# Kernel tuning notes

Hardware: AMD Instinct MI355X
Metric: run time of the kernel (lower is better)

The kernel has to match this reference:

```python
import jax, jax.numpy as jnp
import numpy as np


def pan_conv(x, edge_index, filter_w, lin_w, lin_b):
    """Faithful dense equivalent of PANConv.

    panentropy: pan = w0*I + w1*A + w2*A^2 (filter_size terms).
    PyG then extracts nonzero edges (row=source j, col=target i), computes
    deg = count of pan-edges per row, norm = deg^-1/2[row]*deg^-1/2[col],
    and scatter-adds norm*edge_weight*x_j at target i. Dense form:
      out = d[:,None] * (pan.T @ (d[:,None] * (x @ W.T + b)))
    where d[i] = (row-nnz of pan)^-0.5.
    """
    n = x.shape[0]
    dt = x.dtype
    adj = jnp.zeros((n, n), dt).at[edge_index[0], edge_index[1]].set(1.0)
    eye = jnp.eye(n, dtype=dt)
    pan = filter_w[0] * eye
    tmp = eye
    for i in range(1, filter_w.shape[0]):  # small fixed filter_size loop
        tmp = tmp @ adj
        pan = pan + filter_w[i] * tmp
    # degree() in the original counts edge occurrences = nnz per row of pan
    deg = jnp.sum(pan != 0, axis=1).astype(dt)
    dinv = jnp.where(deg > 0, jax.lax.rsqrt(jnp.maximum(deg, 1.0)), 0.0)
    h = x @ lin_w.T + lin_b  # [n, out_channels]
    return dinv[:, None] * (pan.T @ (dinv[:, None] * h))


def setup_inputs() -> dict:
    key = jax.random.key(0)
    ks = jax.random.split(key, 4)
    N, E, F_IN, H, C = 2048, 32768, 512, 16, 32
    x = jax.random.normal(ks[0], (N, F_IN), jnp.float32)
    edge_index = jax.random.randint(ks[1], (2, E), 0, N, jnp.int32)
    fw1 = 0.1 * jnp.ones(3, jnp.float32)
    fw2 = 0.1 * jnp.ones(3, jnp.float32)
    lin1_w = jax.random.normal(ks[2], (H, F_IN), jnp.float32) / np.sqrt(F_IN).astype(np.float32)
    lin1_b = jnp.zeros(H, jnp.float32)
    lin2_w = jax.random.normal(ks[3], (C, H), jnp.float32) / np.sqrt(H).astype(np.float32)
    lin2_b = jnp.zeros(C, jnp.float32)
    return dict(x=x, edge_index=edge_index, fw1=fw1, lin1_w=lin1_w, lin1_b=lin1_b,
                fw2=fw2, lin2_w=lin2_w, lin2_b=lin2_b)


def reference(x, edge_index, fw1, lin1_w, lin1_b, fw2, lin2_w, lin2_b):
    h = pan_conv(x, edge_index, fw1, lin1_w, lin1_b)
    h = jax.nn.relu(h)  # dropout is identity in eval mode
    h = pan_conv(h, edge_index, fw2, lin2_w, lin2_b)
    return jax.nn.log_softmax(h, axis=1)
```

## Files before the change

### kernel.cpp

```cpp
#include <hip/hip_runtime.h>
#include <hip/hip_bf16.h>

#define NN 2048
#define NW 64

__global__ void k_zero_r9(unsigned* __restrict__ p, int n) {
    int i = blockIdx.x * blockDim.x + threadIdx.x;
    int stride = gridDim.x * blockDim.x;
    for (; i < n; i += stride) p[i] = 0u;
}

__global__ void k_build_r9(const int* __restrict__ ei, int E,
                           unsigned* __restrict__ Abits, unsigned* __restrict__ ATbits) {
    int e = blockIdx.x * blockDim.x + threadIdx.x;
    if (e >= E) return;
    int s = ei[e] & (NN - 1);
    int d = ei[E + e] & (NN - 1);
    atomicOr(&Abits[s * NW + (d >> 5)], 1u << (d & 31));
    atomicOr(&ATbits[d * NW + (s >> 5)], 1u << (s & 31));
}

__global__ void __launch_bounds__(256) k_pandeg_r9(
        const unsigned* __restrict__ Abits,
        const float* __restrict__ fw1, const float* __restrict__ fw2,
        float* __restrict__ dinv1, float* __restrict__ dinv2) {
    __shared__ int cnt[NN];
    __shared__ unsigned rowbits[NW];
    __shared__ int neigh[NN];
    __shared__ int ncnt;
    __shared__ int red1[4], red2[4];

    int i = blockIdx.x, tid = threadIdx.x;
    for (int j = tid; j < NN; j += 256) cnt[j] = 0;
    if (tid < NW) rowbits[tid] = Abits[i * NW + tid];
    if (tid == 0) ncnt = 0;
    __syncthreads();

    if (tid < NW) {
        unsigned bits = rowbits[tid];
        while (bits) {
            int b = __ffs(bits) - 1; bits &= bits - 1;
            int slot = atomicAdd(&ncnt, 1);
            if (slot < NN) neigh[slot] = tid * 32 + b;
        }
    }
    __syncthreads();

    int lane = tid & 63, grp = tid >> 6;
    int nc = ncnt < NN ? ncnt : NN;
    for (int n = grp; n < nc; n += 4) {
        int k = neigh[n];
        unsigned bits = Abits[k * NW + lane];
        while (bits) {
            int b = __ffs(bits) - 1; bits &= bits - 1;
            atomicAdd(&cnt[lane * 32 + b], 1);
        }
    }
    __syncthreads();

    float w10 = fw1[0], w11 = fw1[1], w12 = fw1[2];
    float w20 = fw2[0], w21 = fw2[1], w22 = fw2[2];
    int c1 = 0, c2 = 0;
    for (int j = tid; j < NN; j += 256) {
        float a = ((rowbits[j >> 5] >> (j & 31)) & 1u) ? 1.f : 0.f;
        float c = (float)cnt[j];
        float dg = (j == i) ? 1.f : 0.f;
        c1 += ((w10 * dg + w11 * a + w12 * c) != 0.f);
        c2 += ((w20 * dg + w21 * a + w22 * c) != 0.f);
    }
    for (int o = 32; o; o >>= 1) { c1 += __shfl_down(c1, o); c2 += __shfl_down(c2, o); }
    if (lane == 0) { red1[grp] = c1; red2[grp] = c2; }
    __syncthreads();
    if (tid == 0) {
        int d1 = red1[0] + red1[1] + red1[2] + red1[3];
        int d2 = red2[0] + red2[1] + red2[2] + red2[3];
        dinv1[i] = d1 > 0 ? rsqrtf((float)d1) : 0.f;
        dinv2[i] = d2 > 0 ? rsqrtf((float)d2) : 0.f;
    }
}

__global__ void __launch_bounds__(256) k_lin1_r9(
        const float* __restrict__ x, const float* __restrict__ W,
        const float* __restrict__ b, const float* __restrict__ dinv,
        float* __restrict__ y) {
    __shared__ float xs[528];
    int i = blockIdx.x, tid = threadIdx.x;
    if (tid < 128) {
        float4 v = ((const float4*)(x + i * 512))[tid];
        int f = tid * 4;
        int m = f + (f >> 5);
        xs[m] = v.x; xs[m + 1] = v.y; xs[m + 2] = v.z; xs[m + 3] = v.w;
    }
    __syncthreads();
    int c = tid >> 4, seg = tid & 15;
    const float* wr = W + c * 512 + seg * 32;
    const float* xr = xs + seg * 33;
    float s = 0.f;
#pragma unroll
    for (int f = 0; f < 32; f++) s += xr[f] * wr[f];
    for (int o = 8; o; o >>= 1) s += __shfl_down(s, o, 16);
    if (seg == 0) y[i * 16 + c] = dinv[i] * (s + b[c]);
}

__global__ void __launch_bounds__(256) k_spmm16_r9(
        const unsigned* __restrict__ ATbits, const float* __restrict__ y,
        float* __restrict__ t) {
    __shared__ int neigh[4][64];
    __shared__ int ncnt[4];
    int tid = threadIdx.x, w = tid >> 6, lane = tid & 63;
    int i = blockIdx.x * 4 + w;
    if (lane == 0) ncnt[w] = 0;
    __syncthreads();
    unsigned bits = ATbits[i * NW + lane];
    while (bits) {
        int b = __ffs(bits) - 1; bits &= bits - 1;
        int slot = atomicAdd(&ncnt[w], 1);
        if (slot < 64) neigh[w][slot] = lane * 32 + b;
    }
    __syncthreads();
    int nc = ncnt[w] < 64 ? ncnt[w] : 64;
    int c = lane & 15, grp = lane >> 4;
    float acc = 0.f;
    for (int n = grp; n < nc; n += 4) acc += y[neigh[w][n] * 16 + c];
    acc += __shfl_down(acc, 32);
    acc += __shfl_down(acc, 16);
    if (lane < 16) t[i * 16 + c] = acc;
}

__global__ void __launch_bounds__(256) k_final1_lin2_r9(
        const unsigned* __restrict__ ATbits, const float* __restrict__ y,
        const float* __restrict__ t, const float* __restrict__ dinv1,
        const float* __restrict__ dinv2, const float* __restrict__ fw,
        const float* __restrict__ W2, const float* __restrict__ b2,
        float* __restrict__ y2) {
    __shared__ int neigh[4][64];
    __shared__ int ncnt[4];
    int tid = threadIdx.x, w = tid >> 6, lane = tid & 63;
    int i = blockIdx.x * 4 + w;
    if (lane == 0) ncnt[w] = 0;
    __syncthreads();
    unsigned bits = ATbits[i * NW + lane];
    while (bits) {
        int b = __ffs(bits) - 1; bits &= bits - 1;
        int slot = atomicAdd(&ncnt[w], 1);
        if (slot < 64) neigh[w][slot] = lane * 32 + b;
    }
    __syncthreads();
    int nc = ncnt[w] < 64 ? ncnt[w] : 64;
    int c = lane & 15, grp = lane >> 4;
    float acc = 0.f;
    for (int n = grp; n < nc; n += 4) acc += t[neigh[w][n] * 16 + c];
    acc += __shfl_down(acc, 32);
    acc += __shfl_down(acc, 16);
    float z = fw[0] * y[i * 16 + c] + fw[1] * t[i * 16 + c] + fw[2] * acc;
    z *= dinv1[i];
    z = z > 0.f ? z : 0.f;
    float s2 = 0.f;
#pragma unroll
    for (int f = 0; f < 16; f++) s2 += __shfl(z, f) * W2[lane * 16 + f];
    if (lane < 32) y2[i * 32 + lane] = dinv2[i] * (s2 + b2[lane]);
}

__global__ void __launch_bounds__(256) k_spmm32_r9(
        const unsigned* __restrict__ ATbits, const float* __restrict__ y,
        float* __restrict__ t) {
    __shared__ int neigh[4][64];
    __shared__ int ncnt[4];
    int tid = threadIdx.x, w = tid >> 6, lane = tid & 63;
    int i = blockIdx.x * 4 + w;
    if (lane == 0) ncnt[w] = 0;
    __syncthreads();
    unsigned bits = ATbits[i * NW + lane];
    while (bits) {
        int b = __ffs(bits) - 1; bits &= bits - 1;
        int slot = atomicAdd(&ncnt[w], 1);
        if (slot < 64) neigh[w][slot] = lane * 32 + b;
    }
    __syncthreads();
    int nc = ncnt[w] < 64 ? ncnt[w] : 64;
    int c = lane & 31, grp = lane >> 5;
    float acc = 0.f;
    for (int n = grp; n < nc; n += 2) acc += y[neigh[w][n] * 32 + c];
    acc += __shfl_down(acc, 32);
    if (lane < 32) t[i * 32 + c] = acc;
}

__global__ void __launch_bounds__(256) k_final2_r9(
        const unsigned* __restrict__ ATbits, const float* __restrict__ y,
        const float* __restrict__ t, const float* __restrict__ dinv,
        const float* __restrict__ fw, float* __restrict__ out) {
    __shared__ int neigh[4][64];
    __shared__ int ncnt[4];
    int tid = threadIdx.x, w = tid >> 6, lane = tid & 63;
    int i = blockIdx.x * 4 + w;
    if (lane == 0) ncnt[w] = 0;
    __syncthreads();
    unsigned bits = ATbits[i * NW + lane];
    while (bits) {
        int b = __ffs(bits) - 1; bits &= bits - 1;
        int slot = atomicAdd(&ncnt[w], 1);
        if (slot < 64) neigh[w][slot] = lane * 32 + b;
    }
    __syncthreads();
    int nc = ncnt[w] < 64 ? ncnt[w] : 64;
    int c = lane & 31, grp = lane >> 5;
    float acc = 0.f;
    for (int n = grp; n < nc; n += 2) acc += t[neigh[w][n] * 32 + c];
    acc += __shfl_down(acc, 32);
    float o = dinv[i] * (fw[0] * y[i * 32 + c] + fw[1] * t[i * 32 + c] + fw[2] * acc);
    float m = o;
    for (int k = 16; k; k >>= 1) m = fmaxf(m, __shfl_xor(m, k, 32));
    float e = expf(o - m);
    float ssum = e;
    for (int k = 16; k; k >>= 1) ssum += __shfl_xor(ssum, k, 32);
    if (lane < 32) out[i * 32 + c] = o - m - logf(ssum);
}

extern "C" void kernel_launch(void* const* d_in, const int* in_sizes, int n_in,
                              void* d_out, int out_size, void* d_ws, size_t ws_size,
                              hipStream_t stream) {
    const float* x   = (const float*)d_in[0];
    const int*   ei  = (const int*)d_in[1];
    const float* fw1 = (const float*)d_in[2];
    const float* W1  = (const float*)d_in[3];
    const float* b1  = (const float*)d_in[4];
    const float* fw2 = (const float*)d_in[5];
    const float* W2  = (const float*)d_in[6];
    const float* b2  = (const float*)d_in[7];
    float* out = (float*)d_out;
    int E = in_sizes[1] / 2;

    char* ws = (char*)d_ws;
    size_t off = 0;
    auto alloc = [&](size_t bytes) { void* p = ws + off; off += (bytes + 255) & ~size_t(255); return p; };
    unsigned* Abits  = (unsigned*)alloc(NN * NW * 4);
    unsigned* ATbits = (unsigned*)alloc(NN * NW * 4);
    float* dinv1 = (float*)alloc(NN * 4);
    float* dinv2 = (float*)alloc(NN * 4);
    float* y1 = (float*)alloc(NN * 16 * 4);
    float* t1 = (float*)alloc(NN * 16 * 4);
    float* y2 = (float*)alloc(NN * 32 * 4);
    float* t2 = (float*)alloc(NN * 32 * 4);
    (void)ws_size; (void)n_in; (void)out_size;

    k_zero_r9<<<256, 256, 0, stream>>>(Abits, 2 * NN * NW);
    k_build_r9<<<(E + 255) / 256, 256, 0, stream>>>(ei, E, Abits, ATbits);
    k_pandeg_r9<<<NN, 256, 0, stream>>>(Abits, fw1, fw2, dinv1, dinv2);

    k_lin1_r9<<<NN, 256, 0, stream>>>(x, W1, b1, dinv1, y1);
    k_spmm16_r9<<<NN / 4, 256, 0, stream>>>(ATbits, y1, t1);
    k_final1_lin2_r9<<<NN / 4, 256, 0, stream>>>(ATbits, y1, t1, dinv1, dinv2,
                                                 fw1, W2, b2, y2);
    k_spmm32_r9<<<NN / 4, 256, 0, stream>>>(ATbits, y2, t2);
    k_final2_r9<<<NN / 4, 256, 0, stream>>>(ATbits, y2, t2, dinv2, fw2, out);
}
```

Measured before the change: 110.9 us.

## Fuse all stages into one cooperative persistent kernel with grid syncs

Replaces the eight-kernel pipeline with a single cooperative kernel of 512 blocks, each owning 4 rows, separated by grid.sync barriers. Each block scans the whole edge list to build its own adjacency and transposed rows in shared memory, so the zeroing and global atomic build kernels and the ATbits buffer go away. Degrees, neighbour lists and intermediate values are kept in shared memory across stages. The aim is to remove launch overhead and repeated neighbour-list extraction. In exchange every block rereads all edges, and the kernel now relies on grid-wide barriers and enough occupancy to fit 512 co-resident blocks.

```diff
diff --git a/kernel.cpp b/kernel.cpp
--- a/kernel.cpp
+++ b/kernel.cpp
@@ -1,219 +1,205 @@
 #include <hip/hip_runtime.h>
-#include <hip/hip_bf16.h>
+#include <hip/hip_cooperative_groups.h>
+
+namespace cg = cooperative_groups;
 
 #define NN 2048
 #define NW 64
-
-__global__ void k_zero_r9(unsigned* __restrict__ p, int n) {
-    int i = blockIdx.x * blockDim.x + threadIdx.x;
-    int stride = gridDim.x * blockDim.x;
-    for (; i < n; i += stride) p[i] = 0u;
-}
-
-__global__ void k_build_r9(const int* __restrict__ ei, int E,
-                           unsigned* __restrict__ Abits, unsigned* __restrict__ ATbits) {
-    int e = blockIdx.x * blockDim.x + threadIdx.x;
-    if (e >= E) return;
-    int s = ei[e] & (NN - 1);
-    int d = ei[E + e] & (NN - 1);
-    atomicOr(&Abits[s * NW + (d >> 5)], 1u << (d & 31));
-    atomicOr(&ATbits[d * NW + (s >> 5)], 1u << (s & 31));
-}
-
-__global__ void __launch_bounds__(256) k_pandeg_r9(
-        const unsigned* __restrict__ Abits,
-        const float* __restrict__ fw1, const float* __restrict__ fw2,
-        float* __restrict__ dinv1, float* __restrict__ dinv2) {
-    __shared__ int cnt[NN];
-    __shared__ unsigned rowbits[NW];
-    __shared__ int neigh[NN];
-    __shared__ int ncnt;
-    __shared__ int red1[4], red2[4];
-
-    int i = blockIdx.x, tid = threadIdx.x;
-    for (int j = tid; j < NN; j += 256) cnt[j] = 0;
-    if (tid < NW) rowbits[tid] = Abits[i * NW + tid];
-    if (tid == 0) ncnt = 0;
-    __syncthreads();
-
-    if (tid < NW) {
-        unsigned bits = rowbits[tid];
+#define NBLK 512
+
+__global__ void __launch_bounds__(256, 2) k_mega(
+        const float* __restrict__ x, const int* __restrict__ ei,
+        const float* __restrict__ fw1, const float* __restrict__ W1,
+        const float* __restrict__ b1,
+        const float* __restrict__ fw2, const float* __restrict__ W2,
+        const float* __restrict__ b2,
+        float* __restrict__ out,
+        unsigned* __restrict__ Abits,
+        float* __restrict__ y1, float* __restrict__ t1,
+        float* __restrict__ y2, float* __restrict__ t2,
+        int E)
+{
+    cg::grid_group grid = cg::this_grid();
+
+    __shared__ unsigned Arow[4][NW];
+    __shared__ unsigned ATrow[4][NW];
+    __shared__ int cnt[4][NN];
+    __shared__ int nout[4][128];
+    __shared__ int nin[4][64];
+    __shared__ int noutc[4], ninc[4];
+    __shared__ float xs[528];
+    __shared__ float sdinv1[4], sdinv2[4];
+    __shared__ float sy1[4][16], st1[4][16];
+    __shared__ float sy2[4][32], st2[4][32];
+
+    const int tid = threadIdx.x, blk = blockIdx.x;
+    const int w = tid >> 6, lane = tid & 63;
+    const int i = blk * 4 + w;
+
+    if (tid < 4) { noutc[tid] = 0; ninc[tid] = 0; }
+    (&Arow[0][0])[tid]  = 0u;
+    (&ATrow[0][0])[tid] = 0u;
+    __syncthreads();
+
+    {
+        const int4* s4p = (const int4*)ei;
+        const int4* d4p = (const int4*)(ei + E);
+        const int base = blk << 2;
+#define EDGE_ROW(SS, DD) { \
+        int sv_ = (SS) & (NN - 1), dv_ = (DD) & (NN - 1); \
+        int r_ = sv_ - base; \
+        if ((unsigned)r_ < 4u) atomicOr(&Arow[r_][dv_ >> 5], 1u << (dv_ & 31)); \
+        r_ = dv_ - base; \
+        if ((unsigned)r_ < 4u) atomicOr(&ATrow[r_][sv_ >> 5], 1u << (sv_ & 31)); }
+        for (int e4 = tid; e4 < (E >> 2); e4 += 256) {
+            int4 s4 = s4p[e4], d4 = d4p[e4];
+            EDGE_ROW(s4.x, d4.x)
+            EDGE_ROW(s4.y, d4.y)
+            EDGE_ROW(s4.z, d4.z)
+            EDGE_ROW(s4.w, d4.w)
+        }
+        for (int e = (E & ~3) + tid; e < E; e += 256)
+            EDGE_ROW(ei[e], ei[E + e])
+#undef EDGE_ROW
+    }
+    __syncthreads();
+    Abits[i * NW + lane] = Arow[w][lane];
+    grid.sync();
+
+    {
+        int4 z4 = make_int4(0, 0, 0, 0);
+        int4* c4 = (int4*)cnt[w];
+        for (int t = lane; t < (NN >> 2); t += 64) c4[t] = z4;
+    }
+    {
+        unsigned bits = Arow[w][lane];
         while (bits) {
             int b = __ffs(bits) - 1; bits &= bits - 1;
-            int slot = atomicAdd(&ncnt, 1);
-            if (slot < NN) neigh[slot] = tid * 32 + b;
-        }
-    }
-    __syncthreads();
-
-    int lane = tid & 63, grp = tid >> 6;
-    int nc = ncnt < NN ? ncnt : NN;
-    for (int n = grp; n < nc; n += 4) {
-        int k = neigh[n];
-        unsigned bits = Abits[k * NW + lane];
+            int slot = atomicAdd(&noutc[w], 1);
+            if (slot < 128) nout[w][slot] = lane * 32 + b;
+        }
+    }
+    __syncthreads();
+    const float w10 = fw1[0], w11 = fw1[1], w12 = fw1[2];
+    const float w20 = fw2[0], w21 = fw2[1], w22 = fw2[2];
+    {
+        int nco = noutc[w] < 128 ? noutc[w] : 128;
+        unsigned nxt = 0u;
+        if (nco) nxt = Abits[nout[w][0] * NW + lane];
+        for (int n = 0; n < nco; ++n) {
+            unsigned bits = nxt;
+            if (n + 1 < nco) nxt = Abits[nout[w][n + 1] * NW + lane];
+            while (bits) {
+                int b = __ffs(bits) - 1; bits &= bits - 1;
+                atomicAdd(&cnt[w][lane * 32 + b], 1);
+            }
+        }
+    }
+    int c1 = 0, c2 = 0;
+    for (int it = 0; it < 32; ++it) {
+        int j = it * 64 + lane;
+        float a = ((Arow[w][j >> 5] >> (j & 31)) & 1u) ? 1.f : 0.f;
+        float cp = (float)cnt[w][j];
+        float dg = (j == i) ? 1.f : 0.f;
+        c1 += ((w10 * dg + w11 * a + w12 * cp) != 0.f) ? 1 : 0;
+        c2 += ((w20 * dg + w21 * a + w22 * cp) != 0.f) ? 1 : 0;
+    }
+    for (int o = 32; o; o >>= 1) { c1 += __shfl_xor(c1, o); c2 += __shfl_xor(c2, o); }
+    if (lane == 0) {
+        sdinv1[w] = c1 > 0 ? rsqrtf((float)c1) : 0.f;
+        sdinv2[w] = c2 > 0 ? rsqrtf((float)c2) : 0.f;
+    }
+    {
+        unsigned bits = ATrow[w][lane];
         while (bits) {
             int b = __ffs(bits) - 1; bits &= bits - 1;
-            atomicAdd(&cnt[lane * 32 + b], 1);
-        }
-    }
-    __syncthreads();
-
-    float w10 = fw1[0], w11 = fw1[1], w12 = fw1[2];
-    float w20 = fw2[0], w21 = fw2[1], w22 = fw2[2];
-    int c1 = 0, c2 = 0;
-    for (int j = tid; j < NN; j += 256) {
-        float a = ((rowbits[j >> 5] >> (j & 31)) & 1u) ? 1.f : 0.f;
-        float c = (float)cnt[j];
-        float dg = (j == i) ? 1.f : 0.f;
-        c1 += ((w10 * dg + w11 * a + w12 * c) != 0.f);
-        c2 += ((w20 * dg + w21 * a + w22 * c) != 0.f);
-    }
-    for (int o = 32; o; o >>= 1) { c1 += __shfl_down(c1, o); c2 += __shfl_down(c2, o); }
-    if (lane == 0) { red1[grp] = c1; red2[grp] = c2; }
-    __syncthreads();
-    if (tid == 0) {
-        int d1 = red1[0] + red1[1] + red1[2] + red1[3];
-        int d2 = red2[0] + red2[1] + red2[2] + red2[3];
-        dinv1[i] = d1 > 0 ? rsqrtf((float)d1) : 0.f;
-        dinv2[i] = d2 > 0 ? rsqrtf((float)d2) : 0.f;
-    }
-}
-
-__global__ void __launch_bounds__(256) k_lin1_r9(
-        const float* __restrict__ x, const float* __restrict__ W,
-        const float* __restrict__ b, const float* __restrict__ dinv,
-        float* __restrict__ y) {
-    __shared__ float xs[528];
-    int i = blockIdx.x, tid = threadIdx.x;
-    if (tid < 128) {
-        float4 v = ((const float4*)(x + i * 512))[tid];
-        int f = tid * 4;
-        int m = f + (f >> 5);
-        xs[m] = v.x; xs[m + 1] = v.y; xs[m + 2] = v.z; xs[m + 3] = v.w;
-    }
-    __syncthreads();
-    int c = tid >> 4, seg = tid & 15;
-    const float* wr = W + c * 512 + seg * 32;
-    const float* xr = xs + seg * 33;
-    float s = 0.f;
+            int slot = atomicAdd(&ninc[w], 1);
+            if (slot < 64) nin[w][slot] = lane * 32 + b;
+        }
+    }
+    __syncthreads();
+
+    {
+        int cch = tid >> 4, seg = tid & 15;
+        for (int s = 0; s < 4; ++s) {
+            if (tid < 128) {
+                float4 v = ((const float4*)(x + (blk * 4 + s) * 512))[tid];
+                int f = tid * 4, m = f + (f >> 5);
+                xs[m] = v.x; xs[m + 1] = v.y; xs[m + 2] = v.z; xs[m + 3] = v.w;
+            }
+            __syncthreads();
+            const float* wr = W1 + cch * 512 + seg * 32;
+            const float* xr = xs + seg * 33;
+            float sacc = 0.f;
 #pragma unroll
-    for (int f = 0; f < 32; f++) s += xr[f] * wr[f];
-    for (int o = 8; o; o >>= 1) s += __shfl_down(s, o, 16);
-    if (seg == 0) y[i * 16 + c] = dinv[i] * (s + b[c]);
-}
-
-__global__ void __launch_bounds__(256) k_spmm16_r9(
-        const unsigned* __restrict__ ATbits, const float* __restrict__ y,
-        float* __restrict__ t) {
-    __shared__ int neigh[4][64];
-    __shared__ int ncnt[4];
-    int tid = threadIdx.x, w = tid >> 6, lane = tid & 63;
-    int i = blockIdx.x * 4 + w;
-    if (lane == 0) ncnt[w] = 0;
-    __syncthreads();
-    unsigned bits = ATbits[i * NW + lane];
-    while (bits) {
-        int b = __ffs(bits) - 1; bits &= bits - 1;
-        int slot = atomicAdd(&ncnt[w], 1);
-        if (slot < 64) neigh[w][slot] = lane * 32 + b;
-    }
-    __syncthreads();
-    int nc = ncnt[w] < 64 ? ncnt[w] : 64;
-    int c = lane & 15, grp = lane >> 4;
-    float acc = 0.f;
-    for (int n = grp; n < nc; n += 4) acc += y[neigh[w][n] * 16 + c];
-    acc += __shfl_down(acc, 32);
-    acc += __shfl_down(acc, 16);
-    if (lane < 16) t[i * 16 + c] = acc;
-}
-
-__global__ void __launch_bounds__(256) k_final1_lin2_r9(
-        const unsigned* __restrict__ ATbits, const float* __restrict__ y,
-        const float* __restrict__ t, const float* __restrict__ dinv1,
-        const float* __restrict__ dinv2, const float* __restrict__ fw,
-        const float* __restrict__ W2, const float* __restrict__ b2,
-        float* __restrict__ y2) {
-    __shared__ int neigh[4][64];
-    __shared__ int ncnt[4];
-    int tid = threadIdx.x, w = tid >> 6, lane = tid & 63;
-    int i = blockIdx.x * 4 + w;
-    if (lane == 0) ncnt[w] = 0;
-    __syncthreads();
-    unsigned bits = ATbits[i * NW + lane];
-    while (bits) {
-        int b = __ffs(bits) - 1; bits &= bits - 1;
-        int slot = atomicAdd(&ncnt[w], 1);
-        if (slot < 64) neigh[w][slot] = lane * 32 + b;
-    }
-    __syncthreads();
-    int nc = ncnt[w] < 64 ? ncnt[w] : 64;
-    int c = lane & 15, grp = lane >> 4;
-    float acc = 0.f;
-    for (int n = grp; n < nc; n += 4) acc += t[neigh[w][n] * 16 + c];
-    acc += __shfl_down(acc, 32);
-    acc += __shfl_down(acc, 16);
-    float z = fw[0] * y[i * 16 + c] + fw[1] * t[i * 16 + c] + fw[2] * acc;
-    z *= dinv1[i];
-    z = z > 0.f ? z : 0.f;
-    float s2 = 0.f;
+            for (int f = 0; f < 32; ++f) sacc += xr[f] * wr[f];
+            for (int o = 8; o; o >>= 1) sacc += __shfl_down(sacc, o, 16);
+            if (seg == 0) {
+                float v = sdinv1[s] * (sacc + b1[cch]);
+                y1[(blk * 4 + s) * 16 + cch] = v;
+                sy1[s][cch] = v;
+            }
+            __syncthreads();
+        }
+    }
+    grid.sync();
+
+    const int ncin = ninc[w] < 64 ? ninc[w] : 64;
+    {
+        int c = lane & 15, grp = lane >> 4;
+        float acc = 0.f;
+#pragma unroll 2
+        for (int n = grp; n < ncin; n += 4) acc += y1[nin[w][n] * 16 + c];
+        acc += __shfl_down(acc, 32);
+        acc += __shfl_down(acc, 16);
+        if (lane < 16) { t1[i * 16 + c] = acc; st1[w][c] = acc; }
+    }
+    grid.sync();
+
+    {
+        int c = lane & 15, grp = lane >> 4;
+        float acc = 0.f;
+#pragma unroll 2
+        for (int n = grp; n < ncin; n += 4) acc += t1[nin[w][n] * 16 + c];
+        acc += __shfl_down(acc, 32);
+        acc += __shfl_down(acc, 16);
+        float z = sdinv1[w] * (w10 * sy1[w][c] + w11 * st1[w][c] + w12 * acc);
+        z = z > 0.f ? z : 0.f;
+        float s2 = 0.f;
+        const float* w2r = W2 + (lane & 31) * 16;
 #pragma unroll
-    for (int f = 0; f < 16; f++) s2 += __shfl(z, f) * W2[lane * 16 + f];
-    if (lane < 32) y2[i * 32 + lane] = dinv2[i] * (s2 + b2[lane]);
-}
-
-__global__ void __launch_bounds__(256) k_spmm32_r9(
-        const unsigned* __restrict__ ATbits, const float* __restrict__ y,
-        float* __restrict__ t) {
-    __shared__ int neigh[4][64];
-    __shared__ int ncnt[4];
-    int tid = threadIdx.x, w = tid >> 6, lane = tid & 63;
-    int i = blockIdx.x * 4 + w;
-    if (lane == 0) ncnt[w] = 0;
-    __syncthreads();
-    unsigned bits = ATbits[i * NW + lane];
-    while (bits) {
-        int b = __ffs(bits) - 1; bits &= bits - 1;
-        int slot = atomicAdd(&ncnt[w], 1);
-        if (slot < 64) neigh[w][slot] = lane * 32 + b;
-    }
-    __syncthreads();
-    int nc = ncnt[w] < 64 ? ncnt[w] : 64;
-    int c = lane & 31, grp = lane >> 5;
-    float acc = 0.f;
-    for (int n = grp; n < nc; n += 2) acc += y[neigh[w][n] * 32 + c];
-    acc += __shfl_down(acc, 32);
-    if (lane < 32) t[i * 32 + c] = acc;
-}
-
-__global__ void __launch_bounds__(256) k_final2_r9(
-        const unsigned* __restrict__ ATbits, const float* __restrict__ y,
-        const float* __restrict__ t, const float* __restrict__ dinv,
-        const float* __restrict__ fw, float* __restrict__ out) {
-    __shared__ int neigh[4][64];
-    __shared__ int ncnt[4];
-    int tid = threadIdx.x, w = tid >> 6, lane = tid & 63;
-    int i = blockIdx.x * 4 + w;
-    if (lane == 0) ncnt[w] = 0;
-    __syncthreads();
-    unsigned bits = ATbits[i * NW + lane];
-    while (bits) {
-        int b = __ffs(bits) - 1; bits &= bits - 1;
-        int slot = atomicAdd(&ncnt[w], 1);
-        if (slot < 64) neigh[w][slot] = lane * 32 + b;
-    }
-    __syncthreads();
-    int nc = ncnt[w] < 64 ? ncnt[w] : 64;
-    int c = lane & 31, grp = lane >> 5;
-    float acc = 0.f;
-    for (int n = grp; n < nc; n += 2) acc += t[neigh[w][n] * 32 + c];
-    acc += __shfl_down(acc, 32);
-    float o = dinv[i] * (fw[0] * y[i * 32 + c] + fw[1] * t[i * 32 + c] + fw[2] * acc);
-    float m = o;
-    for (int k = 16; k; k >>= 1) m = fmaxf(m, __shfl_xor(m, k, 32));
-    float e = expf(o - m);
-    float ssum = e;
-    for (int k = 16; k; k >>= 1) ssum += __shfl_xor(ssum, k, 32);
-    if (lane < 32) out[i * 32 + c] = o - m - logf(ssum);
+        for (int f = 0; f < 16; ++f) s2 += __shfl(z, f) * w2r[f];
+        if (lane < 32) {
+            float v = sdinv2[w] * (s2 + b2[lane]);
+            y2[i * 32 + lane] = v; sy2[w][lane] = v;
+        }
+    }
+    grid.sync();
+
+    {
+        int c = lane & 31, grp = lane >> 5;
+        float acc = 0.f;
+#pragma unroll 2
+        for (int n = grp; n < ncin; n += 2) acc += y2[nin[w][n] * 32 + c];
+        acc += __shfl_down(acc, 32);
+        if (lane < 32) { t2[i * 32 + c] = acc; st2[w][c] = acc; }
+    }
+    grid.sync();
+
+    {
+        int c = lane & 31, grp = lane >> 5;
+        float acc = 0.f;
+#pragma unroll 2
+        for (int n = grp; n < ncin; n += 2) acc += t2[nin[w][n] * 32 + c];
+        acc += __shfl_down(acc, 32);
+        float o = sdinv2[w] * (w20 * sy2[w][c] + w21 * st2[w][c] + w22 * acc);
+        float m = o;
+        for (int k = 16; k; k >>= 1) m = fmaxf(m, __shfl_xor(m, k, 32));
+        float e = expf(o - m);
+        float ssum = e;
+        for (int k = 16; k; k >>= 1) ssum += __shfl_xor(ssum, k, 32);
+        if (lane < 32) out[i * 32 + c] = o - m - logf(ssum);
+    }
 }
 
 extern "C" void kernel_launch(void* const* d_in, const int* in_sizes, int n_in,
@@ -233,24 +219,16 @@
     char* ws = (char*)d_ws;
     size_t off = 0;
     auto alloc = [&](size_t bytes) { void* p = ws + off; off += (bytes + 255) & ~size_t(255); return p; };
-    unsigned* Abits  = (unsigned*)alloc(NN * NW * 4);
-    unsigned* ATbits = (unsigned*)alloc(NN * NW * 4);
-    float* dinv1 = (float*)alloc(NN * 4);
-    float* dinv2 = (float*)alloc(NN * 4);
+    unsigned* Abits = (unsigned*)alloc(NN * NW * 4);
     float* y1 = (float*)alloc(NN * 16 * 4);
     float* t1 = (float*)alloc(NN * 16 * 4);
     float* y2 = (float*)alloc(NN * 32 * 4);
     float* t2 = (float*)alloc(NN * 32 * 4);
     (void)ws_size; (void)n_in; (void)out_size;
 
-    k_zero_r9<<<256, 256, 0, stream>>>(Abits, 2 * NN * NW);
-    k_build_r9<<<(E + 255) / 256, 256, 0, stream>>>(ei, E, Abits, ATbits);
-    k_pandeg_r9<<<NN, 256, 0, stream>>>(Abits, fw1, fw2, dinv1, dinv2);
-
-    k_lin1_r9<<<NN, 256, 0, stream>>>(x, W1, b1, dinv1, y1);
-    k_spmm16_r9<<<NN / 4, 256, 0, stream>>>(ATbits, y1, t1);
-    k_final1_lin2_r9<<<NN / 4, 256, 0, stream>>>(ATbits, y1, t1, dinv1, dinv2,
-                                                 fw1, W2, b2, y2);
-    k_spmm32_r9<<<NN / 4, 256, 0, stream>>>(ATbits, y2, t2);
-    k_final2_r9<<<NN / 4, 256, 0, stream>>>(ATbits, y2, t2, dinv2, fw2, out);
+    void* args[] = { (void*)&x, (void*)&ei, (void*)&fw1, (void*)&W1, (void*)&b1,
+                     (void*)&fw2, (void*)&W2, (void*)&b2, (void*)&out,
+                     (void*)&Abits, (void*)&y1, (void*)&t1, (void*)&y2, (void*)&t2,
+                     (void*)&E };
+    hipLaunchCooperativeKernel((void*)k_mega, dim3(NBLK), dim3(256), args, 0, stream);
 }
```

Result: slower. 385.1 us (+247.1%).

## Fuse pipeline into four kernels with per-block adjacency build and two-hop gather

Applied to the files above, without the earlier changes.

Replaces the zero and atomic build kernels with one kernel where each block scans all edges and builds four adjacency rows in shared memory, so no global zeroing or global atomics are needed. Lin1 is fused into the pan-degree kernel. Each layer's SpMM and final step are merged into one per-node kernel that walks two-hop neighbours directly (A^2 applied as A·(A·y)), removing the intermediate t buffers and two launches. The cost is redundant work: every build block reads the full edge list, and the two-hop gathers recompute neighbour sums per target node.

```diff
diff --git a/kernel.cpp b/kernel.cpp
--- a/kernel.cpp
+++ b/kernel.cpp
@@ -1,34 +1,55 @@
 #include <hip/hip_runtime.h>
-#include <hip/hip_bf16.h>
 
 #define NN 2048
 #define NW 64
-
-__global__ void k_zero_r9(unsigned* __restrict__ p, int n) {
-    int i = blockIdx.x * blockDim.x + threadIdx.x;
-    int stride = gridDim.x * blockDim.x;
-    for (; i < n; i += stride) p[i] = 0u;
-}
-
-__global__ void k_build_r9(const int* __restrict__ ei, int E,
-                           unsigned* __restrict__ Abits, unsigned* __restrict__ ATbits) {
-    int e = blockIdx.x * blockDim.x + threadIdx.x;
-    if (e >= E) return;
-    int s = ei[e] & (NN - 1);
-    int d = ei[E + e] & (NN - 1);
-    atomicOr(&Abits[s * NW + (d >> 5)], 1u << (d & 31));
-    atomicOr(&ATbits[d * NW + (s >> 5)], 1u << (s & 31));
-}
-
-__global__ void __launch_bounds__(256) k_pandeg_r9(
+#define BBLK 512
+
+__global__ void __launch_bounds__(256) k_build(const int* __restrict__ ei, int E,
+        unsigned* __restrict__ Abits, unsigned* __restrict__ ATbits) {
+    __shared__ unsigned Arow[4][NW], ATrow[4][NW];
+    int tid = threadIdx.x, blk = blockIdx.x;
+    (&Arow[0][0])[tid]  = 0u;
+    (&ATrow[0][0])[tid] = 0u;
+    __syncthreads();
+    const int4* s4p = (const int4*)ei;
+    const int4* d4p = (const int4*)(ei + E);
+    const int base = blk << 2;
+#define EDGE_ROW(SS, DD) { \
+        int sv_ = (SS) & (NN - 1), dv_ = (DD) & (NN - 1); \
+        int r_ = sv_ - base; \
+        if ((unsigned)r_ < 4u) atomicOr(&Arow[r_][dv_ >> 5], 1u << (dv_ & 31)); \
+        r_ = dv_ - base; \
+        if ((unsigned)r_ < 4u) atomicOr(&ATrow[r_][sv_ >> 5], 1u << (sv_ & 31)); }
+    for (int e4 = tid; e4 < (E >> 2); e4 += 256) {
+        int4 s4 = s4p[e4], d4 = d4p[e4];
+        EDGE_ROW(s4.x, d4.x)
+        EDGE_ROW(s4.y, d4.y)
+        EDGE_ROW(s4.z, d4.z)
+        EDGE_ROW(s4.w, d4.w)
+    }
+    for (int e = (E & ~3) + tid; e < E; e += 256)
+        EDGE_ROW(ei[e], ei[E + e])
+#undef EDGE_ROW
+    __syncthreads();
+    int w = tid >> 6, lane = tid & 63;
+    Abits[(blk * 4 + w) * NW + lane]  = Arow[w][lane];
+    ATbits[(blk * 4 + w) * NW + lane] = ATrow[w][lane];
+}
+
+__global__ void __launch_bounds__(256) k_pandeg_lin1(
         const unsigned* __restrict__ Abits,
         const float* __restrict__ fw1, const float* __restrict__ fw2,
-        float* __restrict__ dinv1, float* __restrict__ dinv2) {
+        const float* __restrict__ x, const float* __restrict__ W1,
+        const float* __restrict__ b1,
+        float* __restrict__ dinv1, float* __restrict__ dinv2,
+        float* __restrict__ y1) {
     __shared__ int cnt[NN];
     __shared__ unsigned rowbits[NW];
     __shared__ int neigh[NN];
     __shared__ int ncnt;
     __shared__ int red1[4], red2[4];
+    __shared__ float xs[528];
+    __shared__ float sd1;
 
     int i = blockIdx.x, tid = threadIdx.x;
     for (int j = tid; j < NN; j += 256) cnt[j] = 0;
@@ -48,12 +69,16 @@
 
     int lane = tid & 63, grp = tid >> 6;
     int nc = ncnt < NN ? ncnt : NN;
-    for (int n = grp; n < nc; n += 4) {
-        int k = neigh[n];
-        unsigned bits = Abits[k * NW + lane];
-        while (bits) {
-            int b = __ffs(bits) - 1; bits &= bits - 1;
-            atomicAdd(&cnt[lane * 32 + b], 1);
+    {
+        int n = grp;
+        unsigned nxt = (n < nc) ? Abits[neigh[n] * NW + lane] : 0u;
+        for (; n < nc; n += 4) {
+            unsigned bits = nxt;
+            if (n + 4 < nc) nxt = Abits[neigh[n + 4] * NW + lane];
+            while (bits) {
+                int b = __ffs(bits) - 1; bits &= bits - 1;
+                atomicAdd(&cnt[lane * 32 + b], 1);
+            }
         }
     }
     __syncthreads();
@@ -74,146 +99,155 @@
     if (tid == 0) {
         int d1 = red1[0] + red1[1] + red1[2] + red1[3];
         int d2 = red2[0] + red2[1] + red2[2] + red2[3];
-        dinv1[i] = d1 > 0 ? rsqrtf((float)d1) : 0.f;
-        dinv2[i] = d2 > 0 ? rsqrtf((float)d2) : 0.f;
-    }
-}
-
-__global__ void __launch_bounds__(256) k_lin1_r9(
-        const float* __restrict__ x, const float* __restrict__ W,
-        const float* __restrict__ b, const float* __restrict__ dinv,
-        float* __restrict__ y) {
-    __shared__ float xs[528];
-    int i = blockIdx.x, tid = threadIdx.x;
+        float v1 = d1 > 0 ? rsqrtf((float)d1) : 0.f;
+        float v2 = d2 > 0 ? rsqrtf((float)d2) : 0.f;
+        dinv1[i] = v1; dinv2[i] = v2; sd1 = v1;
+    }
     if (tid < 128) {
         float4 v = ((const float4*)(x + i * 512))[tid];
-        int f = tid * 4;
-        int m = f + (f >> 5);
+        int f = tid * 4, m = f + (f >> 5);
         xs[m] = v.x; xs[m + 1] = v.y; xs[m + 2] = v.z; xs[m + 3] = v.w;
     }
     __syncthreads();
     int c = tid >> 4, seg = tid & 15;
-    const float* wr = W + c * 512 + seg * 32;
+    const float* wr = W1 + c * 512 + seg * 32;
     const float* xr = xs + seg * 33;
     float s = 0.f;
 #pragma unroll
     for (int f = 0; f < 32; f++) s += xr[f] * wr[f];
     for (int o = 8; o; o >>= 1) s += __shfl_down(s, o, 16);
-    if (seg == 0) y[i * 16 + c] = dinv[i] * (s + b[c]);
-}
-
-__global__ void __launch_bounds__(256) k_spmm16_r9(
-        const unsigned* __restrict__ ATbits, const float* __restrict__ y,
-        float* __restrict__ t) {
-    __shared__ int neigh[4][64];
-    __shared__ int ncnt[4];
-    int tid = threadIdx.x, w = tid >> 6, lane = tid & 63;
-    int i = blockIdx.x * 4 + w;
-    if (lane == 0) ncnt[w] = 0;
-    __syncthreads();
-    unsigned bits = ATbits[i * NW + lane];
-    while (bits) {
-        int b = __ffs(bits) - 1; bits &= bits - 1;
-        int slot = atomicAdd(&ncnt[w], 1);
-        if (slot < 64) neigh[w][slot] = lane * 32 + b;
-    }
-    __syncthreads();
-    int nc = ncnt[w] < 64 ? ncnt[w] : 64;
-    int c = lane & 15, grp = lane >> 4;
-    float acc = 0.f;
-    for (int n = grp; n < nc; n += 4) acc += y[neigh[w][n] * 16 + c];
-    acc += __shfl_down(acc, 32);
-    acc += __shfl_down(acc, 16);
-    if (lane < 16) t[i * 16 + c] = acc;
-}
-
-__global__ void __launch_bounds__(256) k_final1_lin2_r9(
-        const unsigned* __restrict__ ATbits, const float* __restrict__ y,
-        const float* __restrict__ t, const float* __restrict__ dinv1,
+    if (seg == 0) y1[i * 16 + c] = sd1 * (s + b1[c]);
+}
+
+__global__ void __launch_bounds__(256) k_l1tail_lin2(
+        const unsigned* __restrict__ ATbits, const float* __restrict__ y1,
+        const float* __restrict__ dinv1, const float* __restrict__ dinv2,
+        const float* __restrict__ fw, const float* __restrict__ W2,
+        const float* __restrict__ b2, float* __restrict__ y2) {
+    __shared__ int nin[64];
+    __shared__ int nintot;
+    __shared__ int njn[4][64];
+    __shared__ float tacc[4][16], uacc[4][16];
+    __shared__ float hvec[16];
+    int i = blockIdx.x, tid = threadIdx.x, w = tid >> 6, lane = tid & 63;
+
+    if (w == 0) {
+        unsigned bits = ATbits[i * NW + lane];
+        int pc = __popc(bits), incl = pc;
+#pragma unroll
+        for (int o = 1; o < 64; o <<= 1) { int v = __shfl_up(incl, o); if (lane >= o) incl += v; }
+        int slot = incl - pc;
+        if (lane == 63) nintot = incl;
+        while (bits) {
+            int b = __ffs(bits) - 1; bits &= bits - 1;
+            if (slot < 64) nin[slot] = lane * 32 + b;
+            slot++;
+        }
+    }
+    __syncthreads();
+    int ncin = nintot < 64 ? nintot : 64;
+    int c = lane & 15, kg = lane >> 4;
+    float up = 0.f, tp = 0.f;
+    int n = w;
+    unsigned rowbits = (n < ncin) ? ATbits[nin[n] * NW + lane] : 0u;
+    for (; n < ncin; n += 4) {
+        unsigned bits = rowbits;
+        if (n + 4 < ncin) rowbits = ATbits[nin[n + 4] * NW + lane];
+        int pc = __popc(bits), incl = pc;
+#pragma unroll
+        for (int o = 1; o < 64; o <<= 1) { int v = __shfl_up(incl, o); if (lane >= o) incl += v; }
+        int slot = incl - pc;
+        int cnt2 = __shfl(incl, 63);
+        while (bits) {
+            int b = __ffs(bits) - 1; bits &= bits - 1;
+            if (slot < 64) njn[w][slot] = lane * 32 + b;
+            slot++;
+        }
+        cnt2 = cnt2 < 64 ? cnt2 : 64;
+        float tj = 0.f;
+        for (int n2 = kg; n2 < cnt2; n2 += 4) tj += y1[njn[w][n2] * 16 + c];
+        tj += __shfl_down(tj, 32);
+        tj += __shfl_down(tj, 16);
+        if (kg == 0) { up += tj; tp += y1[nin[n] * 16 + c]; }
+    }
+    if (kg == 0) { uacc[w][c] = up; tacc[w][c] = tp; }
+    __syncthreads();
+    if (tid < 16) {
+        float t1i = tacc[0][tid] + tacc[1][tid] + tacc[2][tid] + tacc[3][tid];
+        float ui  = uacc[0][tid] + uacc[1][tid] + uacc[2][tid] + uacc[3][tid];
+        float z = dinv1[i] * (fw[0] * y1[i * 16 + tid] + fw[1] * t1i + fw[2] * ui);
+        hvec[tid] = z > 0.f ? z : 0.f;
+    }
+    __syncthreads();
+    if (tid < 32) {
+        float s2 = 0.f;
+#pragma unroll
+        for (int f = 0; f < 16; f++) s2 += hvec[f] * W2[tid * 16 + f];
+        y2[i * 32 + tid] = dinv2[i] * (s2 + b2[tid]);
+    }
+}
+
+__global__ void __launch_bounds__(256) k_l2tail(
+        const unsigned* __restrict__ ATbits, const float* __restrict__ y2,
         const float* __restrict__ dinv2, const float* __restrict__ fw,
-        const float* __restrict__ W2, const float* __restrict__ b2,
-        float* __restrict__ y2) {
-    __shared__ int neigh[4][64];
-    __shared__ int ncnt[4];
-    int tid = threadIdx.x, w = tid >> 6, lane = tid & 63;
-    int i = blockIdx.x * 4 + w;
-    if (lane == 0) ncnt[w] = 0;
-    __syncthreads();
-    unsigned bits = ATbits[i * NW + lane];
-    while (bits) {
-        int b = __ffs(bits) - 1; bits &= bits - 1;
-        int slot = atomicAdd(&ncnt[w], 1);
-        if (slot < 64) neigh[w][slot] = lane * 32 + b;
-    }
-    __syncthreads();
-    int nc = ncnt[w] < 64 ? ncnt[w] : 64;
-    int c = lane & 15, grp = lane >> 4;
-    float acc = 0.f;
-    for (int n = grp; n < nc; n += 4) acc += t[neigh[w][n] * 16 + c];
-    acc += __shfl_down(acc, 32);
-    acc += __shfl_down(acc, 16);
-    float z = fw[0] * y[i * 16 + c] + fw[1] * t[i * 16 + c] + fw[2] * acc;
-    z *= dinv1[i];
-    z = z > 0.f ? z : 0.f;
-    float s2 = 0.f;
-#pragma unroll
-    for (int f = 0; f < 16; f++) s2 += __shfl(z, f) * W2[lane * 16 + f];
-    if (lane < 32) y2[i * 32 + lane] = dinv2[i] * (s2 + b2[lane]);
-}
-
-__global__ void __launch_bounds__(256) k_spmm32_r9(
-        const unsigned* __restrict__ ATbits, const float* __restrict__ y,
-        float* __restrict__ t) {
-    __shared__ int neigh[4][64];
-    __shared__ int ncnt[4];
-    int tid = threadIdx.x, w = tid >> 6, lane = tid & 63;
-    int i = blockIdx.x * 4 + w;
-    if (lane == 0) ncnt[w] = 0;
-    __syncthreads();
-    unsigned bits = ATbits[i * NW + lane];
-    while (bits) {
-        int b = __ffs(bits) - 1; bits &= bits - 1;
-        int slot = atomicAdd(&ncnt[w], 1);
-        if (slot < 64) neigh[w][slot] = lane * 32 + b;
-    }
-    __syncthreads();
-    int nc = ncnt[w] < 64 ? ncnt[w] : 64;
-    int c = lane & 31, grp = lane >> 5;
-    float acc = 0.f;
-    for (int n = grp; n < nc; n += 2) acc += y[neigh[w][n] * 32 + c];
-    acc += __shfl_down(acc, 32);
-    if (lane < 32) t[i * 32 + c] = acc;
-}
-
-__global__ void __launch_bounds__(256) k_final2_r9(
-        const unsigned* __restrict__ ATbits, const float* __restrict__ y,
-        const float* __restrict__ t, const float* __restrict__ dinv,
-        const float* __restrict__ fw, float* __restrict__ out) {
-    __shared__ int neigh[4][64];
-    __shared__ int ncnt[4];
-    int tid = threadIdx.x, w = tid >> 6, lane = tid & 63;
-    int i = blockIdx.x * 4 + w;
-    if (lane == 0) ncnt[w] = 0;
-    __syncthreads();
-    unsigned bits = ATbits[i * NW + lane];
-    while (bits) {
-        int b = __ffs(bits) - 1; bits &= bits - 1;
-        int slot = atomicAdd(&ncnt[w], 1);
-        if (slot < 64) neigh[w][slot] = lane * 32 + b;
-    }
-    __syncthreads();
-    int nc = ncnt[w] < 64 ? ncnt[w] : 64;
-    int c = lane & 31, grp = lane >> 5;
-    float acc = 0.f;
-    for (int n = grp; n < nc; n += 2) acc += t[neigh[w][n] * 32 + c];
-    acc += __shfl_down(acc, 32);
-    float o = dinv[i] * (fw[0] * y[i * 32 + c] + fw[1] * t[i * 32 + c] + fw[2] * acc);
-    float m = o;
-    for (int k = 16; k; k >>= 1) m = fmaxf(m, __shfl_xor(m, k, 32));
-    float e = expf(o - m);
-    float ssum = e;
-    for (int k = 16; k; k >>= 1) ssum += __shfl_xor(ssum, k, 32);
-    if (lane < 32) out[i * 32 + c] = o - m - logf(ssum);
+        float* __restrict__ out) {
+    __shared__ int nin[64];
+    __shared__ int nintot;
+    __shared__ int njn[4][64];
+    __shared__ float tacc[4][32], uacc[4][32];
+    int i = blockIdx.x, tid = threadIdx.x, w = tid >> 6, lane = tid & 63;
+
+    if (w == 0) {
+        unsigned bits = ATbits[i * NW + lane];
+        int pc = __popc(bits), incl = pc;
+#pragma unroll
+        for (int o = 1; o < 64; o <<= 1) { int v = __shfl_up(incl, o); if (lane >= o) incl += v; }
+        int slot = incl - pc;
+        if (lane == 63) nintot = incl;
+        while (bits) {
+            int b = __ffs(bits) - 1; bits &= bits - 1;
+            if (slot < 64) nin[slot] = lane * 32 + b;
+            slot++;
+        }
+    }
+    __syncthreads();
+    int ncin = nintot < 64 ? nintot : 64;
+    int c = lane & 31, kg = lane >> 5;
+    float up = 0.f, tp = 0.f;
+    int n = w;
+    unsigned rowbits = (n < ncin) ? ATbits[nin[n] * NW + lane] : 0u;
+    for (; n < ncin; n += 4) {
+        unsigned bits = rowbits;
+        if (n + 4 < ncin) rowbits = ATbits[nin[n + 4] * NW + lane];
+        int pc = __popc(bits), incl = pc;
+#pragma unroll
+        for (int o = 1; o < 64; o <<= 1) { int v = __shfl_up(incl, o); if (lane >= o) incl += v; }
+        int slot = incl - pc;
+        int cnt2 = __shfl(incl, 63);
+        while (bits) {
+            int b = __ffs(bits) - 1; bits &= bits - 1;
+            if (slot < 64) njn[w][slot] = lane * 32 + b;
+            slot++;
+        }
+        cnt2 = cnt2 < 64 ? cnt2 : 64;
+        float tj = 0.f;
+        for (int n2 = kg; n2 < cnt2; n2 += 2) tj += y2[njn[w][n2] * 32 + c];
+        tj += __shfl_down(tj, 32);
+        if (kg == 0) { up += tj; tp += y2[nin[n] * 32 + c]; }
+    }
+    if (kg == 0) { uacc[w][c] = up; tacc[w][c] = tp; }
+    __syncthreads();
+    if (tid < 32) {
+        float t2i = tacc[0][tid] + tacc[1][tid] + tacc[2][tid] + tacc[3][tid];
+        float ui  = uacc[0][tid] + uacc[1][tid] + uacc[2][tid] + uacc[3][tid];
+        float o = dinv2[i] * (fw[0] * y2[i * 32 + tid] + fw[1] * t2i + fw[2] * ui);
+        float m = o;
+        for (int k = 16; k; k >>= 1) m = fmaxf(m, __shfl_xor(m, k, 32));
+        float e = expf(o - m);
+        float ssum = e;
+        for (int k = 16; k; k >>= 1) ssum += __shfl_xor(ssum, k, 32);
+        out[i * 32 + tid] = o - m - logf(ssum);
+    }
 }
 
 extern "C" void kernel_launch(void* const* d_in, const int* in_sizes, int n_in,
@@ -238,19 +272,11 @@
     float* dinv1 = (float*)alloc(NN * 4);
     float* dinv2 = (float*)alloc(NN * 4);
     float* y1 = (float*)alloc(NN * 16 * 4);
-    float* t1 = (float*)alloc(NN * 16 * 4);
     float* y2 = (float*)alloc(NN * 32 * 4);
-    float* t2 = (float*)alloc(NN * 32 * 4);
     (void)ws_size; (void)n_in; (void)out_size;
 
-    k_zero_r9<<<256, 256, 0, stream>>>(Abits, 2 * NN * NW);
-    k_build_r9<<<(E + 255) / 256, 256, 0, stream>>>(ei, E, Abits, ATbits);
-    k_pandeg_r9<<<NN, 256, 0, stream>>>(Abits, fw1, fw2, dinv1, dinv2);
-
-    k_lin1_r9<<<NN, 256, 0, stream>>>(x, W1, b1, dinv1, y1);
-    k_spmm16_r9<<<NN / 4, 256, 0, stream>>>(ATbits, y1, t1);
-    k_final1_lin2_r9<<<NN / 4, 256, 0, stream>>>(ATbits, y1, t1, dinv1, dinv2,
-                                                 fw1, W2, b2, y2);
-    k_spmm32_r9<<<NN / 4, 256, 0, stream>>>(ATbits, y2, t2);
-    k_final2_r9<<<NN / 4, 256, 0, stream>>>(ATbits, y2, t2, dinv2, fw2, out);
-}
+    k_build<<<BBLK, 256, 0, stream>>>(ei, E, Abits, ATbits);
+    k_pandeg_lin1<<<NN, 256, 0, stream>>>(Abits, fw1, fw2, x, W1, b1, dinv1, dinv2, y1);
+    k_l1tail_lin2<<<NN, 256, 0, stream>>>(ATbits, y1, dinv1, dinv2, fw1, W2, b2, y2);
+    k_l2tail<<<NN, 256, 0, stream>>>(ATbits, y2, dinv2, fw2, out);
+}
```

Result: slower. 134.7 us (+21.5%).

## Build bitmaps per row block in LDS, fuse lin1 into degree kernel, prefetch rows

Applied to the files above, without the earlier changes.

Replaces the zero and global-atomic build kernels with one kernel where each block owns 16 rows, scans all edges and sets bits in shared memory with LDS atomics, then writes its rows out. The first linear layer is fused into the degree kernel, and the neighbour-row loads in the degree loop are software-prefetched one step ahead. This removes two launches and the global atomics. In exchange, each of the 128 build blocks rereads the full edge list.

```diff
diff --git a/kernel.cpp b/kernel.cpp
--- a/kernel.cpp
+++ b/kernel.cpp
@@ -1,34 +1,58 @@
 #include <hip/hip_runtime.h>
-#include <hip/hip_bf16.h>
 
 #define NN 2048
 #define NW 64
-
-__global__ void k_zero_r9(unsigned* __restrict__ p, int n) {
-    int i = blockIdx.x * blockDim.x + threadIdx.x;
-    int stride = gridDim.x * blockDim.x;
-    for (; i < n; i += stride) p[i] = 0u;
-}
-
-__global__ void k_build_r9(const int* __restrict__ ei, int E,
-                           unsigned* __restrict__ Abits, unsigned* __restrict__ ATbits) {
-    int e = blockIdx.x * blockDim.x + threadIdx.x;
-    if (e >= E) return;
-    int s = ei[e] & (NN - 1);
-    int d = ei[E + e] & (NN - 1);
-    atomicOr(&Abits[s * NW + (d >> 5)], 1u << (d & 31));
-    atomicOr(&ATbits[d * NW + (s >> 5)], 1u << (s & 31));
-}
-
-__global__ void __launch_bounds__(256) k_pandeg_r9(
+#define RB 16
+
+__global__ void __launch_bounds__(256) k_build(const int* __restrict__ ei, int E,
+        unsigned* __restrict__ Abits, unsigned* __restrict__ ATbits) {
+    __shared__ unsigned Arow[RB][NW], ATrow[RB][NW];
+    int tid = threadIdx.x, blk = blockIdx.x;
+    for (int t = tid; t < RB * NW; t += 256) {
+        (&Arow[0][0])[t] = 0u; (&ATrow[0][0])[t] = 0u;
+    }
+    __syncthreads();
+    const int4* s4p = (const int4*)ei;
+    const int4* d4p = (const int4*)(ei + E);
+    const int base = blk * RB;
+#define EDGE_ROW(SS, DD) { \
+        int sv_ = (SS) & (NN - 1), dv_ = (DD) & (NN - 1); \
+        int r_ = sv_ - base; \
+        if ((unsigned)r_ < (unsigned)RB) atomicOr(&Arow[r_][dv_ >> 5], 1u << (dv_ & 31)); \
+        r_ = dv_ - base; \
+        if ((unsigned)r_ < (unsigned)RB) atomicOr(&ATrow[r_][sv_ >> 5], 1u << (sv_ & 31)); }
+    for (int e4 = tid; e4 < (E >> 2); e4 += 256) {
+        int4 s4 = s4p[e4], d4 = d4p[e4];
+        EDGE_ROW(s4.x, d4.x)
+        EDGE_ROW(s4.y, d4.y)
+        EDGE_ROW(s4.z, d4.z)
+        EDGE_ROW(s4.w, d4.w)
+    }
+    for (int e = (E & ~3) + tid; e < E; e += 256)
+        EDGE_ROW(ei[e], ei[E + e])
+#undef EDGE_ROW
+    __syncthreads();
+    int w = tid >> 6, lane = tid & 63;
+    for (int r = w; r < RB; r += 4) {
+        Abits[(blk * RB + r) * NW + lane]  = Arow[r][lane];
+        ATbits[(blk * RB + r) * NW + lane] = ATrow[r][lane];
+    }
+}
+
+__global__ void __launch_bounds__(256) k_pandeg_lin1(
         const unsigned* __restrict__ Abits,
         const float* __restrict__ fw1, const float* __restrict__ fw2,
-        float* __restrict__ dinv1, float* __restrict__ dinv2) {
+        const float* __restrict__ x, const float* __restrict__ W1,
+        const float* __restrict__ b1,
+        float* __restrict__ dinv1, float* __restrict__ dinv2,
+        float* __restrict__ y1) {
     __shared__ int cnt[NN];
     __shared__ unsigned rowbits[NW];
     __shared__ int neigh[NN];
     __shared__ int ncnt;
     __shared__ int red1[4], red2[4];
+    __shared__ float xs[528];
+    __shared__ float sd1;
 
     int i = blockIdx.x, tid = threadIdx.x;
     for (int j = tid; j < NN; j += 256) cnt[j] = 0;
@@ -48,12 +72,16 @@
 
     int lane = tid & 63, grp = tid >> 6;
     int nc = ncnt < NN ? ncnt : NN;
-    for (int n = grp; n < nc; n += 4) {
-        int k = neigh[n];
-        unsigned bits = Abits[k * NW + lane];
-        while (bits) {
-            int b = __ffs(bits) - 1; bits &= bits - 1;
-            atomicAdd(&cnt[lane * 32 + b], 1);
+    {
+        int n = grp;
+        unsigned nxt = (n < nc) ? Abits[neigh[n] * NW + lane] : 0u;
+        for (; n < nc; n += 4) {
+            unsigned bits = nxt;
+            if (n + 4 < nc) nxt = Abits[neigh[n + 4] * NW + lane];
+            while (bits) {
+                int b = __ffs(bits) - 1; bits &= bits - 1;
+                atomicAdd(&cnt[lane * 32 + b], 1);
+            }
         }
     }
     __syncthreads();
@@ -74,35 +102,27 @@
     if (tid == 0) {
         int d1 = red1[0] + red1[1] + red1[2] + red1[3];
         int d2 = red2[0] + red2[1] + red2[2] + red2[3];
-        dinv1[i] = d1 > 0 ? rsqrtf((float)d1) : 0.f;
-        dinv2[i] = d2 > 0 ? rsqrtf((float)d2) : 0.f;
-    }
-}
-
-__global__ void __launch_bounds__(256) k_lin1_r9(
-        const float* __restrict__ x, const float* __restrict__ W,
-        const float* __restrict__ b, const float* __restrict__ dinv,
-        float* __restrict__ y) {
-    __shared__ float xs[528];
-    int i = blockIdx.x, tid = threadIdx.x;
+        float v1 = d1 > 0 ? rsqrtf((float)d1) : 0.f;
+        float v2 = d2 > 0 ? rsqrtf((float)d2) : 0.f;
+        dinv1[i] = v1; dinv2[i] = v2; sd1 = v1;
+    }
     if (tid < 128) {
         float4 v = ((const float4*)(x + i * 512))[tid];
-        int f = tid * 4;
-        int m = f + (f >> 5);
+        int f = tid * 4, m = f + (f >> 5);
         xs[m] = v.x; xs[m + 1] = v.y; xs[m + 2] = v.z; xs[m + 3] = v.w;
     }
     __syncthreads();
     int c = tid >> 4, seg = tid & 15;
-    const float* wr = W + c * 512 + seg * 32;
+    const float* wr = W1 + c * 512 + seg * 32;
     const float* xr = xs + seg * 33;
     float s = 0.f;
 #pragma unroll
     for (int f = 0; f < 32; f++) s += xr[f] * wr[f];
     for (int o = 8; o; o >>= 1) s += __shfl_down(s, o, 16);
-    if (seg == 0) y[i * 16 + c] = dinv[i] * (s + b[c]);
-}
-
-__global__ void __launch_bounds__(256) k_spmm16_r9(
+    if (seg == 0) y1[i * 16 + c] = sd1 * (s + b1[c]);
+}
+
+__global__ void __launch_bounds__(256) k_spmm16(
         const unsigned* __restrict__ ATbits, const float* __restrict__ y,
         float* __restrict__ t) {
     __shared__ int neigh[4][64];
@@ -127,7 +147,7 @@
     if (lane < 16) t[i * 16 + c] = acc;
 }
 
-__global__ void __launch_bounds__(256) k_final1_lin2_r9(
+__global__ void __launch_bounds__(256) k_final1_lin2(
         const unsigned* __restrict__ ATbits, const float* __restrict__ y,
         const float* __restrict__ t, const float* __restrict__ dinv1,
         const float* __restrict__ dinv2, const float* __restrict__ fw,
@@ -161,7 +181,7 @@
     if (lane < 32) y2[i * 32 + lane] = dinv2[i] * (s2 + b2[lane]);
 }
 
-__global__ void __launch_bounds__(256) k_spmm32_r9(
+__global__ void __launch_bounds__(256) k_spmm32(
         const unsigned* __restrict__ ATbits, const float* __restrict__ y,
         float* __restrict__ t) {
     __shared__ int neigh[4][64];
@@ -185,7 +205,7 @@
     if (lane < 32) t[i * 32 + c] = acc;
 }
 
-__global__ void __launch_bounds__(256) k_final2_r9(
+__global__ void __launch_bounds__(256) k_final2(
         const unsigned* __restrict__ ATbits, const float* __restrict__ y,
         const float* __restrict__ t, const float* __restrict__ dinv,
         const float* __restrict__ fw, float* __restrict__ out) {
@@ -243,14 +263,10 @@
     float* t2 = (float*)alloc(NN * 32 * 4);
     (void)ws_size; (void)n_in; (void)out_size;
 
-    k_zero_r9<<<256, 256, 0, stream>>>(Abits, 2 * NN * NW);
-    k_build_r9<<<(E + 255) / 256, 256, 0, stream>>>(ei, E, Abits, ATbits);
-    k_pandeg_r9<<<NN, 256, 0, stream>>>(Abits, fw1, fw2, dinv1, dinv2);
-
-    k_lin1_r9<<<NN, 256, 0, stream>>>(x, W1, b1, dinv1, y1);
-    k_spmm16_r9<<<NN / 4, 256, 0, stream>>>(ATbits, y1, t1);
-    k_final1_lin2_r9<<<NN / 4, 256, 0, stream>>>(ATbits, y1, t1, dinv1, dinv2,
-                                                 fw1, W2, b2, y2);
-    k_spmm32_r9<<<NN / 4, 256, 0, stream>>>(ATbits, y2, t2);
-    k_final2_r9<<<NN / 4, 256, 0, stream>>>(ATbits, y2, t2, dinv2, fw2, out);
-}
+    k_build<<<NN / RB, 256, 0, stream>>>(ei, E, Abits, ATbits);
+    k_pandeg_lin1<<<NN, 256, 0, stream>>>(Abits, fw1, fw2, x, W1, b1, dinv1, dinv2, y1);
+    k_spmm16<<<NN / 4, 256, 0, stream>>>(ATbits, y1, t1);
+    k_final1_lin2<<<NN / 4, 256, 0, stream>>>(ATbits, y1, t1, dinv1, dinv2, fw1, W2, b2, y2);
+    k_spmm32<<<NN / 4, 256, 0, stream>>>(ATbits, y2, t2);
+    k_final2<<<NN / 4, 256, 0, stream>>>(ATbits, y2, t2, dinv2, fw2, out);
+}
```

After: 122.6 us. 1.1x slower.
